# Performance work log

Hardware: AMD Instinct MI355X
Metric: run time of the kernel (lower is better)

Reference implementation:

```python
import jax, jax.numpy as jnp
import numpy as np

IN_FEATURES = 4096
OUT_FEATURES = 4096
GROUP_SIZE = 128
PACKED_COLS = IN_FEATURES // 8
GROUP_COUNT = IN_FEATURES // GROUP_SIZE


def setup_inputs() -> dict:
    key = jax.random.key(0)
    k1, k2, k3, k4 = jax.random.split(key, 4)
    x = jax.random.normal(k1, (4, 2048, IN_FEATURES), dtype=jnp.float32)
    # packed int4 weights: 8 nibbles per int32 word
    qweight = jax.random.randint(k2, (OUT_FEATURES, PACKED_COLS), jnp.iinfo(jnp.int32).min, jnp.iinfo(jnp.int32).max, dtype=jnp.int32)
    qscale = (jax.random.uniform(k3, (GROUP_COUNT, OUT_FEATURES), dtype=jnp.float32) + 0.5) * 0.01
    qzeros = jax.random.randint(k4, (GROUP_COUNT, OUT_FEATURES), 0, 16, dtype=jnp.int32)
    return {"x": x, "qweight": qweight, "qscale": qscale, "qzeros": qzeros}


def _dequantize(qweight, qscale, qzeros):
    out_f, packed_cols = qweight.shape
    in_f = packed_cols * 8
    shifts = jnp.arange(0, 32, 4, dtype=jnp.int32)  # 8 nibbles per int32
    # (out, packed, 8) -> (out, in)
    w_int = ((qweight[:, :, None] >> shifts) & 15).reshape(out_f, in_f).astype(jnp.float32)
    w_int = w_int[:, :IN_FEATURES]
    gids = jnp.arange(IN_FEATURES, dtype=jnp.int32) // GROUP_SIZE  # (in,)
    scales = qscale[gids].T   # (out, in)
    zeros = qzeros[gids].astype(jnp.float32).T  # (out, in)
    return (w_int - zeros) * scales


def reference(x, qweight, qscale, qzeros):
    w = _dequantize(qweight, qscale, qzeros).astype(jnp.bfloat16)  # compute_dtype
    y = jnp.einsum('bsi,oi->bso', x.astype(jnp.bfloat16), w)
    return y.astype(x.dtype)
```

## Files before the change

kernel.cpp:

```cpp
#include <hip/hip_runtime.h>
#include <hip/hip_bf16.h>

#define IN_F   4096
#define OUT_F  4096
#define PACKED (IN_F / 8)
#define M_DIM  8192
#define N_DIM  4096
#define K_DIM  4096

#define BM 256
#define BN 256
#define BK 32
#define NT (K_DIM / BK)

typedef __bf16 bf16x8 __attribute__((ext_vector_type(8)));
typedef float  f32x4  __attribute__((ext_vector_type(4)));

#define BAR() asm volatile("s_barrier" ::: "memory")
#define VMCNT(n) asm volatile("s_waitcnt vmcnt(" #n ")" ::: "memory")
#define AS1 __attribute__((address_space(1)))
#define AS3 __attribute__((address_space(3)))


__global__ __launch_bounds__(256) void dequant_kernel(
    const int* __restrict__ qw, const float* __restrict__ qs,
    const int* __restrict__ qz, __bf16* __restrict__ W)
{
    int ch = blockIdx.x * blockDim.x + threadIdx.x;
    if (ch >= OUT_F * PACKED) return;
    int l     = ch & 63;
    int st    = (ch >> 6) & 15;
    int kTile = (ch >> 10) & 63;
    int nHalf = ch >> 16;
    int o  = nHalf * 128 + ((st >> 1) << 4) + (l & 15);
    int k0 = kTile * 64 + ((st & 1) << 5) + ((l >> 4) << 3);
    int g  = k0 >> 7;
    unsigned int q = (unsigned int)qw[o * PACKED + (k0 >> 3)];
    float scale = qs[g * OUT_F + o];
    float zero  = (float)qz[g * OUT_F + o];
    bf16x8 v;
#pragma unroll
    for (int i = 0; i < 8; ++i) {
        float wi = (float)((q >> (4 * i)) & 15u);
        v[i] = (__bf16)((wi - zero) * scale);
    }
    *reinterpret_cast<bf16x8*>(&W[(size_t)ch * 8]) = v;
}

__global__ __launch_bounds__(256) void cvt_kernel(
    const float* __restrict__ x, __bf16* __restrict__ xb, int nch)
{
    int ch = blockIdx.x * blockDim.x + threadIdx.x;
    if (ch >= nch) return;
    int l     = ch & 63;
    int st    = (ch >> 6) & 15;
    int kTile = (ch >> 10) & 63;
    int mHalf = ch >> 16;
    int m  = mHalf * 128 + ((st >> 1) << 4) + (l & 15);
    int k0 = kTile * 64 + ((st & 1) << 5) + ((l >> 4) << 3);
    const float4* xv = reinterpret_cast<const float4*>(x + (size_t)m * K_DIM + k0);
    float4 a = xv[0];
    float4 b = xv[1];
    bf16x8 v;
    v[0] = (__bf16)a.x; v[1] = (__bf16)a.y; v[2] = (__bf16)a.z; v[3] = (__bf16)a.w;
    v[4] = (__bf16)b.x; v[5] = (__bf16)b.y; v[6] = (__bf16)b.z; v[7] = (__bf16)b.w;
    reinterpret_cast<bf16x8*>(xb)[ch] = v;
}

__global__ __launch_bounds__(512, 2) void gemm_kernel(
    const __bf16* __restrict__ A, const __bf16* __restrict__ B,
    float* __restrict__ C)
{
    extern __shared__ __bf16 lds[];

    const int tid  = threadIdx.x;
    const int lane = tid & 63;
    const int wave = tid >> 6;
    const int wm   = wave >> 2;
    const int wn   = wave & 3;

    const int bid = blockIdx.x;
    const int swz = (bid & 7) * 64 + (bid >> 3);
    const int nBase = (swz & 15) * BN;
    const int mBase = (swz >> 4) * BM;
    const int mHalf = mBase >> 7;
    const int nHalf = nBase >> 7;

    const int lr = lane & 15;

    auto stage_tile = [&](int bufIdx, int t32) {
        __bf16* dst = lds + bufIdx * 16384;
        const int kT = t32 >> 1;
        const int kp = t32 & 1;
#pragma unroll
        for (int i = 0; i < 4; ++i) {
            const int s    = i * 8 + wave;
            const int isB  = (i >> 1);
            const int half = (i & 1);
            const int srcHalf = (isB ? nHalf : mHalf) + half;
            const __bf16* src = (isB ? B : A)
                + ((size_t)(srcHalf * 64 + kT) << 13)
                + (wave * 2 + kp) * 512;
            __builtin_amdgcn_global_load_lds(
                (const AS1 void*)(src + lane * 8),
                (AS3 void*)(dst + s * 512 + lane * 8), 16, 0, 0);
        }
    };

    f32x4 acc[8][4];
#pragma unroll
    for (int i = 0; i < 8; ++i)
#pragma unroll
        for (int j = 0; j < 4; ++j)
            acc[i][j] = 0.0f;

#define LDA(buf, mi) (*(const bf16x8*)((buf) + ((wm * 8 + (mi)) * 512 + lane * 8)))
#define LDB(buf, nj) (*(const bf16x8*)((buf) + 8192 + ((wn * 4 + (nj)) * 512 + lane * 8)))

    stage_tile(0, 0);
    stage_tile(1, 1);
    VMCNT(4);
    BAR();

    for (int t = 0; t < NT; ++t) {
        const __bf16* cur = lds + (t % 3) * 16384;

        if (t + 2 < NT) stage_tile((t + 2) % 3, t + 2);
        __builtin_amdgcn_sched_barrier(0);

        bf16x8 Af[8], Bf[4];
        Af[0] = LDA(cur, 0);
#pragma unroll
        for (int nj = 0; nj < 4; ++nj) Bf[nj] = LDB(cur, nj);
#pragma unroll
        for (int mi = 1; mi < 8; ++mi) Af[mi] = LDA(cur, mi);

#pragma unroll
        for (int mi = 0; mi < 8; ++mi)
#pragma unroll
            for (int nj = 0; nj < 4; ++nj)
                acc[mi][nj] = __builtin_amdgcn_mfma_f32_16x16x32_bf16(
                    Af[mi], Bf[nj], acc[mi][nj], 0, 0, 0);

        if (t < NT - 2)       VMCNT(4);
        else if (t == NT - 2) VMCNT(0);
        BAR();
    }

#pragma unroll
    for (int mi = 0; mi < 8; ++mi)
#pragma unroll
        for (int nj = 0; nj < 4; ++nj) {
            const int col = nBase + wn * 64 + nj * 16 + lr;
#pragma unroll
            for (int r = 0; r < 4; ++r) {
                const int row = mBase + wm * 128 + mi * 16 + (lane >> 4) * 4 + r;
                C[(size_t)row * N_DIM + col] = (float)(__bf16)acc[mi][nj][r];
            }
        }
#undef LDA
#undef LDB
}

extern "C" void kernel_launch(void* const* d_in, const int* in_sizes, int n_in,
                              void* d_out, int out_size, void* d_ws, size_t ws_size,
                              hipStream_t stream)
{
    const float* x       = (const float*)d_in[0];
    const int*   qweight = (const int*)d_in[1];
    const float* qscale  = (const float*)d_in[2];
    const int*   qzeros  = (const int*)d_in[3];
    float*       out     = (float*)d_out;

    __bf16* W  = (__bf16*)d_ws;
    __bf16* xb = (__bf16*)((char*)d_ws + (size_t)N_DIM * K_DIM * sizeof(__bf16));

    {
        int total = OUT_F * PACKED;
        dequant_kernel<<<(total + 255) / 256, 256, 0, stream>>>(qweight, qscale, qzeros, W);
    }
    {
        int nch = (M_DIM * K_DIM) / 8;
        cvt_kernel<<<(nch + 255) / 256, 256, 0, stream>>>(x, xb, nch);
    }
    {
        (void)hipFuncSetAttribute((const void*)gemm_kernel,
                                  hipFuncAttributeMaxDynamicSharedMemorySize, 98304);
        dim3 grid((M_DIM / BM) * (N_DIM / BN));
        gemm_kernel<<<grid, 512, 98304, stream>>>(xb, W, out);
    }
}
```

Before: 292.6 us.

## Stream B fragments from global into registers and phase the GEMM main loop

The GEMM K-tile doubles to 64. Only A is staged through LDS (triple-buffered, in halves). B fragments are now loaded straight from global memory into registers, one tile ahead. Each iteration is split into four MFMA phases with barriers and s_setprio, and the A-half stages and B register prefetches are interleaved between them. The aim is to cut LDS traffic and barrier overhead and to overlap memory with MFMA work. In exchange it adds more barriers, more register pressure, redundant global reads of B across waves, and more delicate vmcnt accounting.

```diff
diff --git a/kernel.cpp b/kernel.cpp
--- a/kernel.cpp
+++ b/kernel.cpp
@@ -10,7 +10,7 @@
 
 #define BM 256
 #define BN 256
-#define BK 32
+#define BK 64
 #define NT (K_DIM / BK)
 
 typedef __bf16 bf16x8 __attribute__((ext_vector_type(8)));
@@ -78,6 +78,9 @@
     const int wave = tid >> 6;
     const int wm   = wave >> 2;
     const int wn   = wave & 3;
+    const int wm8  = wm * 8;
+    const int wn4  = wn * 4;
+    const int lane8 = lane * 8;
 
     const int bid = blockIdx.x;
     const int swz = (bid & 7) * 64 + (bid >> 3);
@@ -88,22 +91,15 @@
 
     const int lr = lane & 15;
 
-    auto stage_tile = [&](int bufIdx, int t32) {
-        __bf16* dst = lds + bufIdx * 16384;
-        const int kT = t32 >> 1;
-        const int kp = t32 & 1;
-#pragma unroll
-        for (int i = 0; i < 4; ++i) {
-            const int s    = i * 8 + wave;
-            const int isB  = (i >> 1);
-            const int half = (i & 1);
-            const int srcHalf = (isB ? nHalf : mHalf) + half;
-            const __bf16* src = (isB ? B : A)
-                + ((size_t)(srcHalf * 64 + kT) << 13)
-                + (wave * 2 + kp) * 512;
+    auto stageA = [&](int t, int h) {
+        __bf16* dst = lds + (t % 3) * 16384 + h * 8192;
+        const __bf16* src = A + ((size_t)((mHalf + h) * 64 + t) << 13);
+#pragma unroll
+        for (int i = 0; i < 2; ++i) {
+            const int st = i * 8 + wave;
             __builtin_amdgcn_global_load_lds(
-                (const AS1 void*)(src + lane * 8),
-                (AS3 void*)(dst + s * 512 + lane * 8), 16, 0, 0);
+                (const AS1 void*)(src + st * 512 + lane8),
+                (AS3 void*)(dst + st * 512 + lane8), 16, 0, 0);
         }
     };
 
@@ -114,36 +110,87 @@
         for (int j = 0; j < 4; ++j)
             acc[i][j] = 0.0f;
 
-#define LDA(buf, mi) (*(const bf16x8*)((buf) + ((wm * 8 + (mi)) * 512 + lane * 8)))
-#define LDB(buf, nj) (*(const bf16x8*)((buf) + 8192 + ((wn * 4 + (nj)) * 512 + lane * 8)))
-
-    stage_tile(0, 0);
-    stage_tile(1, 1);
+    bf16x8 Af[4][2];
+    bf16x8 Bc[4][2];
+
+#define LDA_(cA, mi, kb) (*(const bf16x8*)((cA) + (((wm8 + (mi)) * 2 + (kb)) << 9) + lane8))
+#define LOADB2(njBase, tt) do { \
+    _Pragma("unroll") \
+    for (int _nj = 0; _nj < 2; ++_nj) { \
+        const int _rb = wn4 + (njBase) + _nj; \
+        _Pragma("unroll") \
+        for (int _kb = 0; _kb < 2; ++_kb) { \
+            const __bf16* _p = B + ((size_t)((nHalf + (_rb >> 3)) * 64 + (tt)) << 13) \
+                                 + (((_rb & 7) * 2 + _kb) << 9) + lane8; \
+            Bc[(njBase) + _nj][_kb] = *reinterpret_cast<const bf16x8*>(_p); \
+        } \
+    } \
+} while (0)
+
+    LOADB2(0, 0);
+    LOADB2(2, 0);
+    stageA(0, 0); stageA(0, 1);
+    stageA(1, 0); stageA(1, 1);
     VMCNT(4);
     BAR();
 
     for (int t = 0; t < NT; ++t) {
-        const __bf16* cur = lds + (t % 3) * 16384;
-
-        if (t + 2 < NT) stage_tile((t + 2) % 3, t + 2);
+        const __bf16* cA = lds + (t % 3) * 16384;
+
+#pragma unroll
+        for (int mi = 0; mi < 4; ++mi) { Af[mi][0] = LDA_(cA, mi, 0); Af[mi][1] = LDA_(cA, mi, 1); }
         __builtin_amdgcn_sched_barrier(0);
-
-        bf16x8 Af[8], Bf[4];
-        Af[0] = LDA(cur, 0);
-#pragma unroll
-        for (int nj = 0; nj < 4; ++nj) Bf[nj] = LDB(cur, nj);
-#pragma unroll
-        for (int mi = 1; mi < 8; ++mi) Af[mi] = LDA(cur, mi);
-
-#pragma unroll
-        for (int mi = 0; mi < 8; ++mi)
-#pragma unroll
-            for (int nj = 0; nj < 4; ++nj)
-                acc[mi][nj] = __builtin_amdgcn_mfma_f32_16x16x32_bf16(
-                    Af[mi], Bf[nj], acc[mi][nj], 0, 0, 0);
-
-        if (t < NT - 2)       VMCNT(4);
-        else if (t == NT - 2) VMCNT(0);
+        BAR();
+        __builtin_amdgcn_s_setprio(1);
+#pragma unroll
+        for (int kb = 0; kb < 2; ++kb)
+#pragma unroll
+            for (int mi = 0; mi < 4; ++mi)
+#pragma unroll
+                for (int nj = 0; nj < 2; ++nj)
+                    acc[mi][nj] = __builtin_amdgcn_mfma_f32_16x16x32_bf16(Af[mi][kb], Bc[nj][kb], acc[mi][nj], 0, 0, 0);
+        __builtin_amdgcn_s_setprio(0);
+        BAR();
+
+        if (t < NT - 2) stageA(t + 2, 0);
+        __builtin_amdgcn_sched_barrier(0);
+        BAR();
+        __builtin_amdgcn_s_setprio(1);
+#pragma unroll
+        for (int kb = 0; kb < 2; ++kb)
+#pragma unroll
+            for (int mi = 0; mi < 4; ++mi)
+#pragma unroll
+                for (int nj = 0; nj < 2; ++nj)
+                    acc[mi][nj + 2] = __builtin_amdgcn_mfma_f32_16x16x32_bf16(Af[mi][kb], Bc[nj + 2][kb], acc[mi][nj + 2], 0, 0, 0);
+        __builtin_amdgcn_s_setprio(0);
+        BAR();
+
+#pragma unroll
+        for (int mi = 0; mi < 4; ++mi) { Af[mi][0] = LDA_(cA, mi + 4, 0); Af[mi][1] = LDA_(cA, mi + 4, 1); }
+        if (t < NT - 2) stageA(t + 2, 1);
+        __builtin_amdgcn_sched_barrier(0);
+        BAR();
+        __builtin_amdgcn_s_setprio(1);
+#pragma unroll
+        for (int kb = 0; kb < 2; ++kb)
+#pragma unroll
+            for (int mi = 0; mi < 4; ++mi)
+#pragma unroll
+                for (int nj = 0; nj < 2; ++nj)
+                    acc[mi + 4][nj] = __builtin_amdgcn_mfma_f32_16x16x32_bf16(Af[mi][kb], Bc[nj][kb], acc[mi + 4][nj], 0, 0, 0);
+        if (t < NT - 1) LOADB2(0, t + 1);
+#pragma unroll
+        for (int kb = 0; kb < 2; ++kb)
+#pragma unroll
+            for (int mi = 0; mi < 4; ++mi)
+#pragma unroll
+                for (int nj = 0; nj < 2; ++nj)
+                    acc[mi + 4][nj + 2] = __builtin_amdgcn_mfma_f32_16x16x32_bf16(Af[mi][kb], Bc[nj + 2][kb], acc[mi + 4][nj + 2], 0, 0, 0);
+        if (t < NT - 1) LOADB2(2, t + 1);
+        __builtin_amdgcn_s_setprio(0);
+        if (t < NT - 2)       VMCNT(12);
+        else if (t == NT - 2) VMCNT(8);
         BAR();
     }
 
@@ -158,8 +205,8 @@
                 C[(size_t)row * N_DIM + col] = (float)(__bf16)acc[mi][nj][r];
             }
         }
-#undef LDA
-#undef LDB
+#undef LDA_
+#undef LOADB2
 }
 
 extern "C" void kernel_launch(void* const* d_in, const int* in_sizes, int n_in,
```

Measured after the change: 283.8 us. -3.0%, faster.

## Split GEMM waves into ping-pong gangs with a 4-stage LDS pipeline

Applied to the files above, without the earlier changes.

The GEMM's eight waves are split into two gangs. In each half-iteration one gang reads its fragments from LDS while the other issues its MFMAs, and the roles swap between barriers, so LDS reads and matrix math overlap across waves. MFMA sections raise wave priority with s_setprio. The shared-memory ring grows from three to four stages (128 KB) so three tiles can be prefetched. This costs more LDS and extra barriers, and it depends on the wait-count and barrier ordering being correct for buffer reuse.

```diff
diff --git a/kernel.cpp b/kernel.cpp
--- a/kernel.cpp
+++ b/kernel.cpp
@@ -18,6 +18,7 @@
 
 #define BAR() asm volatile("s_barrier" ::: "memory")
 #define VMCNT(n) asm volatile("s_waitcnt vmcnt(" #n ")" ::: "memory")
+#define LGKM0() asm volatile("s_waitcnt lgkmcnt(0)" ::: "memory")
 #define AS1 __attribute__((address_space(1)))
 #define AS3 __attribute__((address_space(3)))
 
@@ -78,6 +79,8 @@
     const int wave = tid >> 6;
     const int wm   = wave >> 2;
     const int wn   = wave & 3;
+    const bool gangA = (0x69 >> wave) & 1;
+    const int lane8 = lane * 8;
 
     const int bid = blockIdx.x;
     const int swz = (bid & 7) * 64 + (bid >> 3);
@@ -88,8 +91,8 @@
 
     const int lr = lane & 15;
 
-    auto stage_tile = [&](int bufIdx, int t32) {
-        __bf16* dst = lds + bufIdx * 16384;
+    auto stage_tile = [&](int t32) {
+        __bf16* dst = lds + (t32 & 3) * 16384;
         const int kT = t32 >> 1;
         const int kp = t32 & 1;
 #pragma unroll
@@ -102,8 +105,8 @@
                 + ((size_t)(srcHalf * 64 + kT) << 13)
                 + (wave * 2 + kp) * 512;
             __builtin_amdgcn_global_load_lds(
-                (const AS1 void*)(src + lane * 8),
-                (AS3 void*)(dst + s * 512 + lane * 8), 16, 0, 0);
+                (const AS1 void*)(src + lane8),
+                (AS3 void*)(dst + s * 512 + lane8), 16, 0, 0);
         }
     };
 
@@ -114,36 +117,56 @@
         for (int j = 0; j < 4; ++j)
             acc[i][j] = 0.0f;
 
-#define LDA(buf, mi) (*(const bf16x8*)((buf) + ((wm * 8 + (mi)) * 512 + lane * 8)))
-#define LDB(buf, nj) (*(const bf16x8*)((buf) + 8192 + ((wn * 4 + (nj)) * 512 + lane * 8)))
-
-    stage_tile(0, 0);
-    stage_tile(1, 1);
+    bf16x8 fr[12];
+
+#define LDA_(buf, mi) (*(const bf16x8*)((buf) + ((wm * 8 + (mi)) * 512) + lane8))
+#define LDB_(buf, nj) (*(const bf16x8*)((buf) + 8192 + ((wn * 4 + (nj)) * 512) + lane8))
+
+    auto read12 = [&](const __bf16* buf) {
+#pragma unroll
+        for (int mi = 0; mi < 8; ++mi) fr[mi] = LDA_(buf, mi);
+#pragma unroll
+        for (int nj = 0; nj < 4; ++nj) fr[8 + nj] = LDB_(buf, nj);
+    };
+    auto mfma32 = [&]() {
+        __builtin_amdgcn_s_setprio(1);
+#pragma unroll
+        for (int mi = 0; mi < 8; ++mi)
+#pragma unroll
+            for (int nj = 0; nj < 4; ++nj)
+                acc[mi][nj] = __builtin_amdgcn_mfma_f32_16x16x32_bf16(
+                    fr[mi], fr[8 + nj], acc[mi][nj], 0, 0, 0);
+        __builtin_amdgcn_s_setprio(0);
+    };
+
+    stage_tile(0);
+    stage_tile(1);
+    stage_tile(2);
     VMCNT(4);
     BAR();
-
-    for (int t = 0; t < NT; ++t) {
-        const __bf16* cur = lds + (t % 3) * 16384;
-
-        if (t + 2 < NT) stage_tile((t + 2) % 3, t + 2);
+    if (!gangA) read12(lds);
+
+    for (int w = 0; w < NT; ++w) {
+        const __bf16* cur = lds + (w & 3) * 16384;
+
+        if (gangA) {
+            read12(cur);
+            LGKM0();
+            __builtin_amdgcn_sched_barrier(0);
+        } else {
+            mfma32();
+        }
+        BAR();
+
+        if (w + 3 < NT) stage_tile(w + 3);
         __builtin_amdgcn_sched_barrier(0);
-
-        bf16x8 Af[8], Bf[4];
-        Af[0] = LDA(cur, 0);
-#pragma unroll
-        for (int nj = 0; nj < 4; ++nj) Bf[nj] = LDB(cur, nj);
-#pragma unroll
-        for (int mi = 1; mi < 8; ++mi) Af[mi] = LDA(cur, mi);
-
-#pragma unroll
-        for (int mi = 0; mi < 8; ++mi)
-#pragma unroll
-            for (int nj = 0; nj < 4; ++nj)
-                acc[mi][nj] = __builtin_amdgcn_mfma_f32_16x16x32_bf16(
-                    Af[mi], Bf[nj], acc[mi][nj], 0, 0, 0);
-
-        if (t < NT - 2)       VMCNT(4);
-        else if (t == NT - 2) VMCNT(0);
+        if (gangA) {
+            mfma32();
+        } else {
+            if (w + 1 < NT) read12(lds + ((w + 1) & 3) * 16384);
+        }
+        if (w + 4 < NT) { VMCNT(4); }
+        else           { VMCNT(0); }
         BAR();
     }
 
@@ -158,8 +181,8 @@
                 C[(size_t)row * N_DIM + col] = (float)(__bf16)acc[mi][nj][r];
             }
         }
-#undef LDA
-#undef LDB
+#undef LDA_
+#undef LDB_
 }
 
 extern "C" void kernel_launch(void* const* d_in, const int* in_sizes, int n_in,
@@ -185,8 +208,8 @@
     }
     {
         (void)hipFuncSetAttribute((const void*)gemm_kernel,
-                                  hipFuncAttributeMaxDynamicSharedMemorySize, 98304);
+                                  hipFuncAttributeMaxDynamicSharedMemorySize, 131072);
         dim3 grid((M_DIM / BM) * (N_DIM / BN));
-        gemm_kernel<<<grid, 512, 98304, stream>>>(xb, W, out);
-    }
-}
+        gemm_kernel<<<grid, 512, 131072, stream>>>(xb, W, out);
+    }
+}
```

Result: no change. 294.5 us (+0.7%).
